# Kernel optimization log

Measured on AMD Instinct MI355X. Metric: run time of the kernel, lower is better.

The kernel has to match this reference:

```python
import jax, jax.numpy as jnp
import numpy as np

EPS = 1e-5
NUM_GROUPS = 32


def setup_inputs() -> dict:
    key = jax.random.key(0)
    ks = jax.random.split(key, 4)
    b, c, h, w = 8, 512, 32, 32
    x = jax.random.normal(ks[0], (b, c, h, w), dtype=jnp.float32)
    gn_weight = jnp.ones((c,), dtype=jnp.float32)
    gn_bias = jnp.zeros((c,), dtype=jnp.float32)
    qkv_w = jax.random.normal(ks[1], (3 * c, c), dtype=jnp.float32) * (1.0 / np.sqrt(c))
    qkv_b = jnp.zeros((3 * c,), dtype=jnp.float32)
    proj_w = jax.random.normal(ks[2], (c, c), dtype=jnp.float32) * (1.0 / np.sqrt(c))
    proj_b = jnp.zeros((c,), dtype=jnp.float32)
    return {"x": x, "gn_weight": gn_weight, "gn_bias": gn_bias,
            "qkv_w": qkv_w, "qkv_b": qkv_b, "proj_w": proj_w, "proj_b": proj_b}


def _group_norm(x, weight, bias):
    b, c, h, w = x.shape
    xg = x.reshape(b, NUM_GROUPS, c // NUM_GROUPS, h, w)
    mean = xg.mean(axis=(2, 3, 4), keepdims=True)
    var = xg.var(axis=(2, 3, 4), keepdims=True)
    xn = ((xg - mean) * jax.lax.rsqrt(var + EPS)).reshape(b, c, h, w)
    return xn * weight[None, :, None, None] + bias[None, :, None, None]


def reference(x, gn_weight, gn_bias, qkv_w, qkv_b, proj_w, proj_b):
    b, c, h, w = x.shape
    scale = c ** (-0.5)
    xn = _group_norm(x, gn_weight, gn_bias)
    # 1x1 conv == per-pixel matmul over channels
    qkv = jnp.einsum('bchw,oc->bohw', xn, qkv_w) + qkv_b[None, :, None, None]
    q, k, v = jnp.split(qkv.reshape(b, 3 * c, h * w), 3, axis=1)  # each [b, c, N]
    attn = jax.nn.softmax(jnp.einsum('bci,bcj->bij', q, k) * scale, axis=-1)
    out = jnp.einsum('bij,bcj->bci', attn, v).reshape(b, c, h, w)
    proj = jnp.einsum('bchw,oc->bohw', out, proj_w) + proj_b[None, :, None, None]
    return x + proj
```

## Files before the change

### kernel.cpp

```cpp
#include <hip/hip_runtime.h>
#include <hip/hip_fp16.h>
#include <cmath>

constexpr int Bsz = 8, Cch = 512, NPIX = 1024;
constexpr int NG = 32, CPG = 16;

typedef __attribute__((ext_vector_type(4))) float f32x4;
typedef __attribute__((ext_vector_type(8))) short s16x8;

#define GLOBAL_AS __attribute__((address_space(1)))
#define LDS_AS __attribute__((address_space(3)))

__device__ inline short f2bf(float f) {
  union { float f; unsigned u; } c = {f};
  unsigned r = (c.u + 0x7fffu + ((c.u >> 16) & 1u)) >> 16;
  return (short)r;
}

__device__ inline float wave_reduce_sum(float v) {
#pragma unroll
  for (int off = 32; off > 0; off >>= 1) v += __shfl_xor(v, off, 64);
  return v;
}
__device__ inline float wave_reduce_max(float v) {
#pragma unroll
  for (int off = 32; off > 0; off >>= 1) v = fmaxf(v, __shfl_xor(v, off, 64));
  return v;
}

__global__ __launch_bounds__(256) void prep_kernel(
    const float* __restrict__ x, const float* __restrict__ w,
    const float* __restrict__ bb, short* __restrict__ xnt,
    const float* __restrict__ in1, short* __restrict__ out1, int n1,
    const float* __restrict__ in2, short* __restrict__ out2, int n2) {
  __shared__ float sm[8];
  if (blockIdx.x >= 256) {
    const int i = ((blockIdx.x - 256) * 256 + threadIdx.x) * 4;
    const float* in = in1;
    short* out = out1;
    int j = i;
    if (i >= n1) { in = in2; out = out2; j = i - n1; }
    if (j + 3 < (i >= n1 ? n2 : n1)) {
      float4 v = *(const float4*)(in + j);
      short o[4] = {f2bf(v.x), f2bf(v.y), f2bf(v.z), f2bf(v.w)};
      *(uint2*)(out + j) = *(const uint2*)o;
    }
    return;
  }
  const int bg = blockIdx.x, b = bg >> 5, g = bg & 31;
  const float* xp = x + ((size_t)(b * Cch + g * CPG)) * NPIX;
  float s = 0.f, ss = 0.f;
  for (int i = threadIdx.x * 4; i < CPG * NPIX; i += 1024) {
    float4 v = *(const float4*)(xp + i);
    s += v.x + v.y + v.z + v.w;
    ss += v.x * v.x + v.y * v.y + v.z * v.z + v.w * v.w;
  }
  s = wave_reduce_sum(s);
  ss = wave_reduce_sum(ss);
  const int wv = threadIdx.x >> 6;
  if ((threadIdx.x & 63) == 0) { sm[wv] = s; sm[4 + wv] = ss; }
  __syncthreads();
  const float tsum = sm[0] + sm[1] + sm[2] + sm[3];
  const float tsq = sm[4] + sm[5] + sm[6] + sm[7];
  const float inv_n = 1.0f / (CPG * NPIX);
  const float mean = tsum * inv_n;
  const float rstd = rsqrtf(tsq * inv_n - mean * mean + 1e-5f);
  float wc[CPG], bc[CPG];
#pragma unroll
  for (int c = 0; c < CPG; ++c) {
    wc[c] = w[g * CPG + c] * rstd;
    bc[c] = bb[g * CPG + c] - mean * wc[c];
  }
  for (int p = threadIdx.x; p < NPIX; p += 256) {
    short ov[CPG];
#pragma unroll
    for (int c = 0; c < CPG; ++c)
      ov[c] = f2bf(xp[(size_t)c * NPIX + p] * wc[c] + bc[c]);
    short* op = xnt + ((size_t)(b * NPIX + p)) * Cch + g * CPG;
    *(uint4*)op = *(const uint4*)&ov[0];
    *(uint4*)(op + 8) = *(const uint4*)&ov[8];
  }
}

template <int BM, int BN, int EPI>
__global__ __launch_bounds__(256) void mfma_gemm(
    const short* __restrict__ A, const short* __restrict__ B, int K, int lda,
    int ldb, long sA, long sB, const float* __restrict__ bias, float alpha,
    void* __restrict__ Cp, long sC, int ldc, void* __restrict__ C2p, long sC2,
    const float* __restrict__ resid, long sR) {
  constexpr int FM = BM / 32, FN = BN / 32;
  constexpr int NA = BM / 32, NB = BN / 32;
  __shared__ __align__(16) short Asl[BM * 64];
  __shared__ __align__(16) short Bsl[BN * 64];
  const int t = threadIdx.x;
  const int lane = t & 63, wave = t >> 6;
  const int bz = blockIdx.z;
  const int m0 = blockIdx.y * BM, n0 = blockIdx.x * BN;
  A += sA * bz;
  B += sB * bz;

  const short* ga[NA];
  const short* gb[NB];
  short* la[NA];
  short* lb[NB];
#pragma unroll
  for (int i = 0; i < NA; ++i) {
    const int c = i * 256 + t;
    const int row = ((c >> 7) << 4) + (c & 15);
    const int koff = ((c >> 6) & 1) * 32 + ((c >> 4) & 3) * 8;
    ga[i] = A + (size_t)(m0 + row) * lda + koff;
    la[i] = Asl + c * 8;
  }
#pragma unroll
  for (int i = 0; i < NB; ++i) {
    const int c = i * 256 + t;
    const int row = ((c >> 7) << 4) + (c & 15);
    const int koff = ((c >> 6) & 1) * 32 + ((c >> 4) & 3) * 8;
    gb[i] = B + (size_t)(n0 + row) * ldb + koff;
    lb[i] = Bsl + c * 8;
  }

  f32x4 acc[FM][FN] = {};
  const int wm = wave & 1, wn = wave >> 1;

  for (int k0 = 0; k0 < K; k0 += 64) {
#pragma unroll
    for (int i = 0; i < NA; ++i) {
      __builtin_amdgcn_global_load_lds((const GLOBAL_AS void*)ga[i],
                                       (LDS_AS void*)la[i], 16, 0, 0);
      ga[i] += 64;
    }
#pragma unroll
    for (int i = 0; i < NB; ++i) {
      __builtin_amdgcn_global_load_lds((const GLOBAL_AS void*)gb[i],
                                       (LDS_AS void*)lb[i], 16, 0, 0);
      gb[i] += 64;
    }
    __syncthreads();
#pragma unroll
    for (int p = 0; p < 2; ++p) {
      s16x8 af[FM], bf[FN];
#pragma unroll
      for (int i = 0; i < FM; ++i)
        af[i] = *(const s16x8*)(Asl + (wm * FM + i) * 1024 + p * 512 + lane * 8);
#pragma unroll
      for (int i = 0; i < FN; ++i)
        bf[i] = *(const s16x8*)(Bsl + (wn * FN + i) * 1024 + p * 512 + lane * 8);
#pragma unroll
      for (int im = 0; im < FM; ++im)
#pragma unroll
        for (int in = 0; in < FN; ++in)
          acc[im][in] = __builtin_amdgcn_mfma_f32_16x16x32_bf16(
              af[im], bf[in], acc[im][in], 0, 0, 0);
    }
    __syncthreads();
  }

  const int quad = lane >> 4, nn = lane & 15;
#pragma unroll
  for (int im = 0; im < FM; ++im) {
#pragma unroll
    for (int in = 0; in < FN; ++in) {
      const int m = m0 + (wm * FM + im) * 16 + quad * 4;
      const int n = n0 + (wn * FN + in) * 16 + nn;
      if (EPI == 0) {
        if (m0 < 1024) {
          short* Cq = (short*)Cp + sC * bz;
          short o[4];
#pragma unroll
          for (int r = 0; r < 4; ++r) o[r] = f2bf(acc[im][in][r] + bias[m + r]);
          *(uint2*)(Cq + (size_t)n * ldc + m) = *(const uint2*)o;
        } else {
          short* Cv = (short*)C2p + sC2 * bz;
#pragma unroll
          for (int r = 0; r < 4; ++r)
            Cv[(size_t)(m - 1024 + r) * ldc + n] =
                f2bf(acc[im][in][r] + bias[m + r]);
        }
      } else if (EPI == 1) {
        __half* Ch = (__half*)Cp + sC * bz;
#pragma unroll
        for (int r = 0; r < 4; ++r)
          Ch[(size_t)(m + r) * ldc + n] = __float2half(acc[im][in][r] * alpha);
      } else if (EPI == 2) {
        short* Cs = (short*)Cp + sC * bz;
#pragma unroll
        for (int r = 0; r < 4; ++r)
          Cs[(size_t)(m + r) * ldc + n] = f2bf(acc[im][in][r]);
      } else {
        float* Cf = (float*)Cp + sC * bz;
        const float* R = resid + sR * bz;
#pragma unroll
        for (int r = 0; r < 4; ++r)
          Cf[(size_t)(m + r) * ldc + n] =
              acc[im][in][r] + bias[m + r] + R[(size_t)(m + r) * ldc + n];
      }
    }
  }
}

__global__ __launch_bounds__(256) void softmax_kernel(const __half* __restrict__ S,
                                                      short* __restrict__ P) {
  __shared__ float sm[8];
  const __half* p = S + (size_t)blockIdx.x * 1024;
  const int t = threadIdx.x;
  uint2 raw = ((const uint2*)p)[t];
  __half2 h0 = *(const __half2*)&raw.x, h1 = *(const __half2*)&raw.y;
  float2 f0 = __half22float2(h0), f1 = __half22float2(h1);
  float4 v = {f0.x, f0.y, f1.x, f1.y};
  float mx = fmaxf(fmaxf(v.x, v.y), fmaxf(v.z, v.w));
  mx = wave_reduce_max(mx);
  if ((t & 63) == 0) sm[t >> 6] = mx;
  __syncthreads();
  mx = fmaxf(fmaxf(sm[0], sm[1]), fmaxf(sm[2], sm[3]));
  v.x = __expf(v.x - mx);
  v.y = __expf(v.y - mx);
  v.z = __expf(v.z - mx);
  v.w = __expf(v.w - mx);
  float s = v.x + v.y + v.z + v.w;
  s = wave_reduce_sum(s);
  if ((t & 63) == 0) sm[4 + (t >> 6)] = s;
  __syncthreads();
  const float inv = 1.0f / (sm[4] + sm[5] + sm[6] + sm[7]);
  short o[4] = {f2bf(v.x * inv), f2bf(v.y * inv), f2bf(v.z * inv),
                f2bf(v.w * inv)};
  *(uint2*)(P + (size_t)blockIdx.x * 1024 + t * 4) = *(const uint2*)o;
}

extern "C" void kernel_launch(void* const* d_in, const int* in_sizes, int n_in,
                              void* d_out, int out_size, void* d_ws,
                              size_t ws_size, hipStream_t stream) {
  const float* x = (const float*)d_in[0];
  const float* gnw = (const float*)d_in[1];
  const float* gnb = (const float*)d_in[2];
  const float* qkvw = (const float*)d_in[3];
  const float* qkvb = (const float*)d_in[4];
  const float* projw = (const float*)d_in[5];
  const float* projb = (const float*)d_in[6];
  float* out = (float*)d_out;

  char* ws = (char*)d_ws;
  short* xnt = (short*)ws;
  short* qkt = (short*)(ws + (8ull << 20));
  short* vbuf = (short*)(ws + (24ull << 20));
  __half* Sbuf = (__half*)(ws + (32ull << 20));
  short* Pbuf = (short*)(ws + (64ull << 20));
  short* Ot = (short*)(ws + (80ull << 20));
  short* wq = (short*)(ws + (88ull << 20));
  short* wp = (short*)(ws + (89ull << 20) + (512ull << 10));

  prep_kernel<<<1280, 256, 0, stream>>>(x, gnw, gnb, xnt, qkvw, wq, 1536 * 512,
                                        projw, wp, 512 * 512);

  mfma_gemm<128, 128, 0><<<dim3(8, 12, Bsz), 256, 0, stream>>>(
      wq, xnt, 512, 512, 512, 0L, 1024L * 512, qkvb, 1.0f, qkt, 1024L * 1024,
      1024, vbuf, 512L * 1024, nullptr, 0L);

  const float scale = 1.0f / sqrtf(512.0f);
  mfma_gemm<128, 128, 1><<<dim3(8, 8, Bsz), 256, 0, stream>>>(
      qkt, qkt + 512, 512, 1024, 1024, 1024L * 1024, 1024L * 1024, nullptr,
      scale, Sbuf, 1024L * 1024, 1024, nullptr, 0L, nullptr, 0L);

  softmax_kernel<<<Bsz * 1024, 256, 0, stream>>>(Sbuf, Pbuf);

  mfma_gemm<128, 64, 2><<<dim3(8, 8, Bsz), 256, 0, stream>>>(
      Pbuf, vbuf, 1024, 1024, 1024, 1024L * 1024, 512L * 1024, nullptr, 1.0f,
      Ot, 1024L * 512, 512, nullptr, 0L, nullptr, 0L);

  mfma_gemm<64, 128, 3><<<dim3(8, 8, Bsz), 256, 0, stream>>>(
      wp, Ot, 512, 512, 512, 0L, 1024L * 512, projb, 1.0f, out, 512L * 1024,
      1024, nullptr, 0L, x, 512L * 1024);
}
```

Baseline: 205.3 us.

## Double-buffer LDS tiles in MFMA GEMM to overlap global loads with compute

Doubles the shared-memory A and B tile buffers and restructures the K loop to prefetch the next 64-wide K slice into the alternate buffer while MFMAs consume the current one. This drops one of the two barriers per iteration and is meant to hide global-to-LDS load latency behind matrix math. The cost is twice the LDS per block, which can lower occupancy. Correctness depends on the single remaining barrier, which must make the asynchronous global_load_lds writes visible before the next iteration reads them.

After: 211.9 us. +3.2%, slower.

```diff
diff --git a/kernel.cpp b/kernel.cpp
--- a/kernel.cpp
+++ b/kernel.cpp
@@ -90,8 +90,9 @@
     const float* __restrict__ resid, long sR) {
   constexpr int FM = BM / 32, FN = BN / 32;
   constexpr int NA = BM / 32, NB = BN / 32;
-  __shared__ __align__(16) short Asl[BM * 64];
-  __shared__ __align__(16) short Bsl[BN * 64];
+  constexpr int ABUF = BM * 64, BBUF = BN * 64;
+  __shared__ __align__(16) short Asl[2 * ABUF];
+  __shared__ __align__(16) short Bsl[2 * BBUF];
   const int t = threadIdx.x;
   const int lane = t & 63, wave = t >> 6;
   const int bz = blockIdx.z;
@@ -123,29 +124,72 @@
   f32x4 acc[FM][FN] = {};
   const int wm = wave & 1, wn = wave >> 1;
 
-  for (int k0 = 0; k0 < K; k0 += 64) {
+#pragma unroll
+  for (int i = 0; i < NA; ++i) {
+    __builtin_amdgcn_global_load_lds((const GLOBAL_AS void*)ga[i],
+                                     (LDS_AS void*)la[i], 16, 0, 0);
+    ga[i] += 64;
+  }
+#pragma unroll
+  for (int i = 0; i < NB; ++i) {
+    __builtin_amdgcn_global_load_lds((const GLOBAL_AS void*)gb[i],
+                                     (LDS_AS void*)lb[i], 16, 0, 0);
+    gb[i] += 64;
+  }
+  __syncthreads();
+
+  int cur = 0;
+  for (int k0 = 64; k0 < K; k0 += 64) {
+    const int nxt = cur ^ 1;
 #pragma unroll
     for (int i = 0; i < NA; ++i) {
       __builtin_amdgcn_global_load_lds((const GLOBAL_AS void*)ga[i],
-                                       (LDS_AS void*)la[i], 16, 0, 0);
+                                       (LDS_AS void*)(la[i] + nxt * ABUF), 16,
+                                       0, 0);
       ga[i] += 64;
     }
 #pragma unroll
     for (int i = 0; i < NB; ++i) {
       __builtin_amdgcn_global_load_lds((const GLOBAL_AS void*)gb[i],
-                                       (LDS_AS void*)lb[i], 16, 0, 0);
+                                       (LDS_AS void*)(lb[i] + nxt * BBUF), 16,
+                                       0, 0);
       gb[i] += 64;
     }
+    {
+      const short* Ab = Asl + cur * ABUF;
+      const short* Bb = Bsl + cur * BBUF;
+#pragma unroll
+      for (int p = 0; p < 2; ++p) {
+        s16x8 af[FM], bf[FN];
+#pragma unroll
+        for (int i = 0; i < FM; ++i)
+          af[i] = *(const s16x8*)(Ab + (wm * FM + i) * 1024 + p * 512 + lane * 8);
+#pragma unroll
+        for (int i = 0; i < FN; ++i)
+          bf[i] = *(const s16x8*)(Bb + (wn * FN + i) * 1024 + p * 512 + lane * 8);
+#pragma unroll
+        for (int im = 0; im < FM; ++im)
+#pragma unroll
+          for (int in = 0; in < FN; ++in)
+            acc[im][in] = __builtin_amdgcn_mfma_f32_16x16x32_bf16(
+                af[im], bf[in], acc[im][in], 0, 0, 0);
+      }
+    }
     __syncthreads();
+    cur = nxt;
+  }
+  {
+    const short* Ab = Asl + cur * ABUF;
+    const short* Bb = Bsl + cur * BBUF;
 #pragma unroll
     for (int p = 0; p < 2; ++p) {
       s16x8 af[FM], bf[FN];
 #pragma unroll
       for (int i = 0; i < FM; ++i)
-        af[i] = *(const s16x8*)(Asl + (wm * FM + i) * 1024 + p * 512 + lane * 8);
+        af[i] = *(const s16x8*)(Ab + (wm * FM + i) * 1024 + p * 512 + lane * 8);
 #pragma unroll
       for (int i = 0; i < FN; ++i)
-        bf[i] = *(const s16x8*)(Bsl + (wn * FN + i) * 1024 + p * 512 + lane * 8);
+        bf[i] = *(const s16x8*)(Bb + (wn * FN + i) * 1024 + p * 512 + lane * 8);
 #pragma unroll
       for (int im = 0; im < FM; ++im)
 #pragma unroll
@@ -153,7 +197,6 @@
           acc[im][in] = __builtin_amdgcn_mfma_f32_16x16x32_bf16(
               af[im], bf[in], acc[im][in], 0, 0, 0);
     }
-    __syncthreads();
   }
 
   const int quad = lane >> 4, nn = lane & 15;
```
